# Kernel optimization log

Measured on AMD Instinct MI355X. Metric: run time of the kernel, lower is better.

## Reference

```python
import jax, jax.numpy as jnp
import numpy as np

T = 1000      # self.length in DMM
B = 16384     # batch
Z_DIM, X_DIM, H_DIM = 2, 3, 2
SIGMA = 0.01  # fixed scale used in both model and guide Normals
LOG2PI = float(np.log(2.0 * np.pi))


def _normal_logprob(x, mu, sigma):
    # elementwise Normal(mu, sigma).log_prob(x)
    return -0.5 * jnp.square((x - mu) / sigma) - jnp.log(sigma) - 0.5 * LOG2PI


def setup_inputs() -> dict:
    key = jax.random.key(0)
    ks = jax.random.split(key, 12)
    s = 0.3  # modest init scale for tiny linears
    return {
        "data": jax.random.normal(ks[0], (T, B, X_DIM), dtype=jnp.float32),
        "eps":  jax.random.normal(ks[1], (T, B, Z_DIM), dtype=jnp.float32),
        # guide RNN (Elman, tanh): input 3 -> hidden 2
        "W_ih": jax.random.normal(ks[2], (H_DIM, X_DIM), dtype=jnp.float32) * s,
        "W_hh": jax.random.normal(ks[3], (H_DIM, H_DIM), dtype=jnp.float32) * s,
        "b_ih": jax.random.normal(ks[4], (H_DIM,), dtype=jnp.float32) * s,
        "b_hh": jax.random.normal(ks[5], (H_DIM,), dtype=jnp.float32) * s,
        "h0":   jnp.zeros((H_DIM,), dtype=jnp.float32),   # nn.Parameter h_0
        "z0":   jnp.zeros((Z_DIM,), dtype=jnp.float32),   # nn.Parameter z_0
        # transition: Linear(2,2)
        "Wt": jax.random.normal(ks[6], (Z_DIM, Z_DIM), dtype=jnp.float32) * s,
        "bt": jax.random.normal(ks[7], (Z_DIM,), dtype=jnp.float32) * s,
        # emission: Linear(2,3)
        "We": jax.random.normal(ks[8], (X_DIM, Z_DIM), dtype=jnp.float32) * s,
        "be": jax.random.normal(ks[9], (X_DIM,), dtype=jnp.float32) * s,
    }


def reference(data, eps, W_ih, W_hh, b_ih, b_hh, h0, z0, Wt, bt, We, be):
    """Guide RNN + reparameterized latents + model log-joint minus guide log-prob.

    data: [T, B, 3], eps: [T, B, 2]. Returns scalar ELBO-style objective.
    """
    batch = data.shape[1]

    # --- guide: RNN over data (sequential recurrence, lax.scan) ---
    def step(h, x_t):
        h_new = jnp.tanh(x_t @ W_ih.T + b_ih + h @ W_hh.T + b_hh)
        return h_new, h_new

    h0b = jnp.broadcast_to(h0, (batch, H_DIM))
    _, rnn_out = jax.lax.scan(step, h0b, data)            # [T, B, 2]

    # z_t = Normal(rnn_out[t-1], SIGMA) sample, t = 1..T-1 (reparameterized)
    q_loc = rnn_out[:-1]                                   # [T-1, B, 2]
    z = q_loc + SIGMA * eps[1:]                            # [T-1, B, 2]

    # --- model: transition + emission over the latent chain ---
    z_prev = jnp.concatenate(
        [jnp.broadcast_to(z0, (1, batch, Z_DIM)), z[:-1]], axis=0)  # [T-1, B, 2]
    z_loc = z_prev @ Wt.T + bt                             # transition mean
    x_loc = z @ We.T + be                                  # emission mean [T-1, B, 3]

    logp = (_normal_logprob(z, z_loc, SIGMA).sum()
            + _normal_logprob(data[1:], x_loc, SIGMA).sum())
    logq = _normal_logprob(z, q_loc, SIGMA).sum()
    return logp - logq
```

## Files before the change

### kernel.cpp

```cpp
#include <hip/hip_runtime.h>

#define T_STEPS 1000
#define BATCH   16384

#define CH      40
#define NCHUNK  25
#define WARM    20
#define TT      4
#define BLK     256
#define NPART   (NCHUNK * (BATCH / BLK))

struct P {
    float w00,w01,w02,w10,w11,w12;
    float u00,u01,u10,u11,bs0,bs1;
    float wt00,wt01,wt10,wt11,bt0,bt1;
    float we00,we01,we10,we11,we20,we21,be0,be1,be2;
};

__device__ __forceinline__ float fast_tanh(float x) {
    float e = __expf(2.0f * x);
    return 1.0f - __fdividef(2.0f, e + 1.0f);
}

__device__ __forceinline__ void rnn_step(const P& p, float X0, float X1, float X2,
                                         float& h0, float& h1) {
    float p0 = p.bs0;
    p0 = __fmaf_rn(p.w00, X0, p0);
    p0 = __fmaf_rn(p.w01, X1, p0);
    p0 = __fmaf_rn(p.w02, X2, p0);
    p0 = __fmaf_rn(p.u00, h0, p0);
    p0 = __fmaf_rn(p.u01, h1, p0);
    float p1 = p.bs1;
    p1 = __fmaf_rn(p.w10, X0, p1);
    p1 = __fmaf_rn(p.w11, X1, p1);
    p1 = __fmaf_rn(p.w12, X2, p1);
    p1 = __fmaf_rn(p.u10, h0, p1);
    p1 = __fmaf_rn(p.u11, h1, p1);
    h0 = fast_tanh(p0);
    h1 = fast_tanh(p1);
}

__device__ __forceinline__ void body(const P& p, float X0, float X1, float X2,
                                     float E0, float E1,
                                     float& h0, float& h1, float& zp0, float& zp1,
                                     float& ssq, float& esq) {
    const float z0 = __fmaf_rn(0.01f, E0, h0);
    const float z1 = __fmaf_rn(0.01f, E1, h1);
    const float zl0 = __fmaf_rn(p.wt00, zp0, __fmaf_rn(p.wt01, zp1, p.bt0));
    const float zl1 = __fmaf_rn(p.wt10, zp0, __fmaf_rn(p.wt11, zp1, p.bt1));
    const float xl0 = __fmaf_rn(p.we00, z0, __fmaf_rn(p.we01, z1, p.be0));
    const float xl1 = __fmaf_rn(p.we10, z0, __fmaf_rn(p.we11, z1, p.be1));
    const float xl2 = __fmaf_rn(p.we20, z0, __fmaf_rn(p.we21, z1, p.be2));
    const float r0 = z0 - zl0;
    const float r1 = z1 - zl1;
    const float r2 = X0 - xl0;
    const float r3 = X1 - xl1;
    const float r4 = X2 - xl2;
    float s = r0 * r0;
    s = __fmaf_rn(r1, r1, s);
    s = __fmaf_rn(r2, r2, s);
    s = __fmaf_rn(r3, r3, s);
    s = __fmaf_rn(r4, r4, s);
    ssq += s;
    esq = __fmaf_rn(E0, E0, esq);
    esq = __fmaf_rn(E1, E1, esq);
    zp0 = z0; zp1 = z1;
    rnn_step(p, X0, X1, X2, h0, h1);
}

template<bool EPS_>
__device__ __forceinline__ void stage_tile(const float* __restrict__ data,
        const float* __restrict__ eps, float* db, float* ebf,
        int tbase, int b0, int w, int lane)
{
    const float4* srcd = reinterpret_cast<const float4*>(
        data + ((size_t)(tbase + w) * BATCH + b0) * 3);
    float4* dd = reinterpret_cast<float4*>(db + w * (BLK * 3));
    dd[lane]       = srcd[lane];
    dd[lane + 64]  = srcd[lane + 64];
    dd[lane + 128] = srcd[lane + 128];
    if constexpr (EPS_) {
        const float4* srce = reinterpret_cast<const float4*>(
            eps + ((size_t)(tbase + w) * BATCH + b0) * 2);
        float4* de = reinterpret_cast<float4*>(ebf + w * (BLK * 2));
        de[lane]      = srce[lane];
        de[lane + 64] = srce[lane + 64];
    }
}

template<int NW, bool TR, int NB>
__device__ __forceinline__ void compute_tile(const P& p, const float* db,
        const float* ebf, int tid,
        float& h0, float& h1, float& zp0, float& zp1, float& ssq, float& esq)
{
    const float* dp = db + tid * 3;
    const float2* ep = reinterpret_cast<const float2*>(ebf) + tid;
    int s = 0;
#pragma unroll
    for (int i = 0; i < NW; ++i, ++s)
        rnn_step(p, dp[s*BLK*3 + 0], dp[s*BLK*3 + 1], dp[s*BLK*3 + 2], h0, h1);
    if constexpr (TR) {
        const float2 E = ep[s * BLK];
        zp0 = __fmaf_rn(0.01f, E.x, h0);
        zp1 = __fmaf_rn(0.01f, E.y, h1);
        rnn_step(p, dp[s*BLK*3 + 0], dp[s*BLK*3 + 1], dp[s*BLK*3 + 2], h0, h1);
        ++s;
    }
#pragma unroll
    for (int i = 0; i < NB; ++i, ++s) {
        const float2 E = ep[s * BLK];
        body(p, dp[s*BLK*3 + 0], dp[s*BLK*3 + 1], dp[s*BLK*3 + 2],
             E.x, E.y, h0, h1, zp0, zp1, ssq, esq);
    }
}

template<int NT, int TRK, int TR_NW, int TR_NB, int EPS_FROM>
__device__ __forceinline__ void run_tiles(
    const float* __restrict__ data, const float* __restrict__ eps,
    float* dls0, float* dls1, float* els0, float* els1,
    int tb, int b0, int w, int lane, int tid, const P& p,
    float& h0, float& h1, float& zp0, float& zp1, float& ssq, float& esq)
{
    if (0 >= EPS_FROM) stage_tile<true >(data, eps, dls0, els0, tb, b0, w, lane);
    else               stage_tile<false>(data, eps, dls0, els0, tb, b0, w, lane);
    __syncthreads();
#pragma unroll
    for (int k = 0; k < NT; ++k) {
        float* dcur = (k & 1) ? dls1 : dls0;
        float* ecur = (k & 1) ? els1 : els0;
        float* dnxt = (k & 1) ? dls0 : dls1;
        float* enxt = (k & 1) ? els0 : els1;
        if (k + 1 < NT) {
            if ((k + 1) >= EPS_FROM)
                stage_tile<true >(data, eps, dnxt, enxt, tb + (k + 1) * TT, b0, w, lane);
            else
                stage_tile<false>(data, eps, dnxt, enxt, tb + (k + 1) * TT, b0, w, lane);
        }
        if (k < TRK)
            compute_tile<TT, false, 0>(p, dcur, ecur, tid, h0, h1, zp0, zp1, ssq, esq);
        else if (k == TRK)
            compute_tile<TR_NW, true, TR_NB>(p, dcur, ecur, tid, h0, h1, zp0, zp1, ssq, esq);
        else
            compute_tile<0, false, TT>(p, dcur, ecur, tid, h0, h1, zp0, zp1, ssq, esq);
        __syncthreads();
    }
}

__global__ __launch_bounds__(BLK, 2)
void elbo_kernel(const float* __restrict__ data,
                 const float* __restrict__ eps,
                 const float* __restrict__ W_ih,
                 const float* __restrict__ W_hh,
                 const float* __restrict__ b_ih,
                 const float* __restrict__ b_hh,
                 const float* __restrict__ h0p,
                 const float* __restrict__ z0p,
                 const float* __restrict__ Wt,
                 const float* __restrict__ bt,
                 const float* __restrict__ We,
                 const float* __restrict__ be,
                 float* __restrict__ partial)
{
    __shared__ float dls0[TT * BLK * 3], dls1[TT * BLK * 3];
    __shared__ float els0[TT * BLK * 2], els1[TT * BLK * 2];

    const int tid  = threadIdx.x;
    const int w    = tid >> 6;
    const int lane = tid & 63;
    const int b0   = blockIdx.x * BLK;
    const int b    = b0 + tid;
    const int c    = blockIdx.y;

    P p;
    p.w00 = W_ih[0]; p.w01 = W_ih[1]; p.w02 = W_ih[2];
    p.w10 = W_ih[3]; p.w11 = W_ih[4]; p.w12 = W_ih[5];
    p.u00 = W_hh[0]; p.u01 = W_hh[1]; p.u10 = W_hh[2]; p.u11 = W_hh[3];
    p.bs0 = b_ih[0] + b_hh[0];
    p.bs1 = b_ih[1] + b_hh[1];
    p.wt00 = Wt[0]; p.wt01 = Wt[1]; p.wt10 = Wt[2]; p.wt11 = Wt[3];
    p.bt0 = bt[0]; p.bt1 = bt[1];
    p.we00 = We[0]; p.we01 = We[1];
    p.we10 = We[2]; p.we11 = We[3];
    p.we20 = We[4]; p.we21 = We[5];
    p.be0 = be[0]; p.be1 = be[1]; p.be2 = be[2];

    float h0 = h0p[0], h1 = h0p[1];
    float zp0 = z0p[0], zp1 = z0p[1];
    float ssq = 0.0f, esq = 0.0f;

    if (c == 0) {
        const float* d0 = data + (size_t)b * 3;
        rnn_step(p, d0[0], d0[1], d0[2], h0, h1);
        run_tiles<10, -1, 0, 3, 0>(data, eps, dls0, dls1, els0, els1,
                                   1, b0, w, lane, tid, p, h0, h1, zp0, zp1, ssq, esq);
    } else if (c < NCHUNK - 1) {
        const int tp = c * CH - WARM;
        const float* dpr = data + ((size_t)tp * BATCH + b) * 3;
        rnn_step(p, dpr[0], dpr[1], dpr[2], h0, h1);
        run_tiles<15, 4, 3, 0, 4>(data, eps, dls0, dls1, els0, els1,
                                  tp + 1, b0, w, lane, tid, p, h0, h1, zp0, zp1, ssq, esq);
    } else {
        run_tiles<15, 5, 0, 3, 5>(data, eps, dls0, dls1, els0, els1,
                                  (NCHUNK - 1) * CH - WARM, b0, w, lane, tid, p,
                                  h0, h1, zp0, zp1, ssq, esq);
    }

    const int na = (c < NCHUNK - 1) ? CH : (T_STEPS - 1 - (NCHUNK - 1) * CH);
    const float CPT = (float)na * (3.0f * 3.6862316527806026f);
    float tval = __fmaf_rn(ssq, -5000.0f, __fmaf_rn(esq, 0.5f, CPT));

#pragma unroll
    for (int off = 32; off >= 1; off >>= 1)
        tval += __shfl_down(tval, off, 64);

    __shared__ float sm[BLK / 64];
    if ((tid & 63) == 0) sm[tid >> 6] = tval;
    __syncthreads();
    if (tid == 0) {
        float s = sm[0];
#pragma unroll
        for (int j = 1; j < BLK / 64; ++j) s += sm[j];
        partial[c * (BATCH / BLK) + blockIdx.x] = s;
    }
}

__global__ __launch_bounds__(256)
void reduce_kernel(const float* __restrict__ partial, float* __restrict__ out)
{
    float s = 0.0f;
    for (int i = threadIdx.x; i < NPART; i += 256)
        s += partial[i];
    __shared__ float sm[4];
#pragma unroll
    for (int off = 32; off >= 1; off >>= 1)
        s += __shfl_down(s, off, 64);
    if ((threadIdx.x & 63) == 0) sm[threadIdx.x >> 6] = s;
    __syncthreads();
    if (threadIdx.x == 0)
        out[0] = sm[0] + sm[1] + sm[2] + sm[3];
}

extern "C" void kernel_launch(void* const* d_in, const int* in_sizes, int n_in,
                              void* d_out, int out_size, void* d_ws, size_t ws_size,
                              hipStream_t stream) {
    const float* data = (const float*)d_in[0];
    const float* eps  = (const float*)d_in[1];
    const float* W_ih = (const float*)d_in[2];
    const float* W_hh = (const float*)d_in[3];
    const float* b_ih = (const float*)d_in[4];
    const float* b_hh = (const float*)d_in[5];
    const float* h0   = (const float*)d_in[6];
    const float* z0   = (const float*)d_in[7];
    const float* Wt   = (const float*)d_in[8];
    const float* bt   = (const float*)d_in[9];
    const float* We   = (const float*)d_in[10];
    const float* be   = (const float*)d_in[11];
    float* out     = (float*)d_out;
    float* partial = (float*)d_ws;

    elbo_kernel<<<dim3(BATCH / BLK, NCHUNK), dim3(BLK), 0, stream>>>(
        data, eps, W_ih, W_hh, b_ih, b_hh, h0, z0, Wt, bt, We, be, partial);
    reduce_kernel<<<dim3(1), dim3(256), 0, stream>>>(partial, out);
}
```

Baseline: 382.7 us.

## Prefetch next tile into registers and write LDS after compute; raise occupancy

Replaces the fully unrolled, templated per-chunk tile loop with a single runtime loop. The next tile's global loads go into registers before the current tile is computed, and are written to shared memory only after compute. This lets global load latency hide behind compute instead of stalling on the direct global-to-LDS copy. The change also raises launch_bounds min blocks from 2 to 3 and merges the three code paths to cut code size. In exchange it adds staging registers, a runtime-branching transition tile, and a tighter register budget that could cause spills.

```diff
diff --git a/kernel.cpp b/kernel.cpp
--- a/kernel.cpp
+++ b/kernel.cpp
@@ -68,85 +68,90 @@
     rnn_step(p, X0, X1, X2, h0, h1);
 }
 
-template<bool EPS_>
-__device__ __forceinline__ void stage_tile(const float* __restrict__ data,
-        const float* __restrict__ eps, float* db, float* ebf,
-        int tbase, int b0, int w, int lane)
+struct Stg {
+    float4 d0, d1, d2;
+    float4 e0, e1;
+};
+
+__device__ __forceinline__ void stage_load(const float* __restrict__ data,
+        const float* __restrict__ eps, Stg& r,
+        int tbase, int b0, int w, int lane, bool do_eps)
 {
     const float4* srcd = reinterpret_cast<const float4*>(
         data + ((size_t)(tbase + w) * BATCH + b0) * 3);
-    float4* dd = reinterpret_cast<float4*>(db + w * (BLK * 3));
-    dd[lane]       = srcd[lane];
-    dd[lane + 64]  = srcd[lane + 64];
-    dd[lane + 128] = srcd[lane + 128];
-    if constexpr (EPS_) {
+    r.d0 = srcd[lane];
+    r.d1 = srcd[lane + 64];
+    r.d2 = srcd[lane + 128];
+    if (do_eps) {
         const float4* srce = reinterpret_cast<const float4*>(
             eps + ((size_t)(tbase + w) * BATCH + b0) * 2);
+        r.e0 = srce[lane];
+        r.e1 = srce[lane + 64];
+    }
+}
+
+__device__ __forceinline__ void stage_write(float* db, float* ebf, const Stg& r,
+        int w, int lane, bool do_eps)
+{
+    float4* dd = reinterpret_cast<float4*>(db + w * (BLK * 3));
+    dd[lane]       = r.d0;
+    dd[lane + 64]  = r.d1;
+    dd[lane + 128] = r.d2;
+    if (do_eps) {
         float4* de = reinterpret_cast<float4*>(ebf + w * (BLK * 2));
-        de[lane]      = srce[lane];
-        de[lane + 64] = srce[lane + 64];
-    }
-}
-
-template<int NW, bool TR, int NB>
-__device__ __forceinline__ void compute_tile(const P& p, const float* db,
+        de[lane]      = r.e0;
+        de[lane + 64] = r.e1;
+    }
+}
+
+__device__ __forceinline__ void compute_warm4(const P& p, const float* db, int tid,
+        float& h0, float& h1)
+{
+    const float* dp = db + tid * 3;
+#pragma unroll
+    for (int s = 0; s < TT; ++s)
+        rnn_step(p, dp[s*BLK*3 + 0], dp[s*BLK*3 + 1], dp[s*BLK*3 + 2], h0, h1);
+}
+
+__device__ __forceinline__ void compute_body4(const P& p, const float* db,
         const float* ebf, int tid,
         float& h0, float& h1, float& zp0, float& zp1, float& ssq, float& esq)
 {
     const float* dp = db + tid * 3;
     const float2* ep = reinterpret_cast<const float2*>(ebf) + tid;
-    int s = 0;
-#pragma unroll
-    for (int i = 0; i < NW; ++i, ++s)
-        rnn_step(p, dp[s*BLK*3 + 0], dp[s*BLK*3 + 1], dp[s*BLK*3 + 2], h0, h1);
-    if constexpr (TR) {
-        const float2 E = ep[s * BLK];
-        zp0 = __fmaf_rn(0.01f, E.x, h0);
-        zp1 = __fmaf_rn(0.01f, E.y, h1);
-        rnn_step(p, dp[s*BLK*3 + 0], dp[s*BLK*3 + 1], dp[s*BLK*3 + 2], h0, h1);
-        ++s;
-    }
-#pragma unroll
-    for (int i = 0; i < NB; ++i, ++s) {
+#pragma unroll
+    for (int s = 0; s < TT; ++s) {
         const float2 E = ep[s * BLK];
         body(p, dp[s*BLK*3 + 0], dp[s*BLK*3 + 1], dp[s*BLK*3 + 2],
              E.x, E.y, h0, h1, zp0, zp1, ssq, esq);
     }
 }
 
-template<int NT, int TRK, int TR_NW, int TR_NB, int EPS_FROM>
-__device__ __forceinline__ void run_tiles(
-    const float* __restrict__ data, const float* __restrict__ eps,
-    float* dls0, float* dls1, float* els0, float* els1,
-    int tb, int b0, int w, int lane, int tid, const P& p,
-    float& h0, float& h1, float& zp0, float& zp1, float& ssq, float& esq)
-{
-    if (0 >= EPS_FROM) stage_tile<true >(data, eps, dls0, els0, tb, b0, w, lane);
-    else               stage_tile<false>(data, eps, dls0, els0, tb, b0, w, lane);
-    __syncthreads();
-#pragma unroll
-    for (int k = 0; k < NT; ++k) {
-        float* dcur = (k & 1) ? dls1 : dls0;
-        float* ecur = (k & 1) ? els1 : els0;
-        float* dnxt = (k & 1) ? dls0 : dls1;
-        float* enxt = (k & 1) ? els0 : els1;
-        if (k + 1 < NT) {
-            if ((k + 1) >= EPS_FROM)
-                stage_tile<true >(data, eps, dnxt, enxt, tb + (k + 1) * TT, b0, w, lane);
-            else
-                stage_tile<false>(data, eps, dnxt, enxt, tb + (k + 1) * TT, b0, w, lane);
+__device__ __forceinline__ void compute_tr(const P& p, const float* db,
+        const float* ebf, int tid, int nw,
+        float& h0, float& h1, float& zp0, float& zp1, float& ssq, float& esq)
+{
+    const float* dp = db + tid * 3;
+    const float2* ep = reinterpret_cast<const float2*>(ebf) + tid;
+    for (int s = 0; s < TT; ++s) {
+        const float X0 = dp[s*BLK*3 + 0];
+        const float X1 = dp[s*BLK*3 + 1];
+        const float X2 = dp[s*BLK*3 + 2];
+        if (s < nw) {
+            rnn_step(p, X0, X1, X2, h0, h1);
+        } else if (s == nw) {
+            const float2 E = ep[s * BLK];
+            zp0 = __fmaf_rn(0.01f, E.x, h0);
+            zp1 = __fmaf_rn(0.01f, E.y, h1);
+            rnn_step(p, X0, X1, X2, h0, h1);
+        } else {
+            const float2 E = ep[s * BLK];
+            body(p, X0, X1, X2, E.x, E.y, h0, h1, zp0, zp1, ssq, esq);
         }
-        if (k < TRK)
-            compute_tile<TT, false, 0>(p, dcur, ecur, tid, h0, h1, zp0, zp1, ssq, esq);
-        else if (k == TRK)
-            compute_tile<TR_NW, true, TR_NB>(p, dcur, ecur, tid, h0, h1, zp0, zp1, ssq, esq);
-        else
-            compute_tile<0, false, TT>(p, dcur, ecur, tid, h0, h1, zp0, zp1, ssq, esq);
-        __syncthreads();
-    }
-}
-
-__global__ __launch_bounds__(BLK, 2)
+    }
+}
+
+__global__ __launch_bounds__(BLK, 3)
 void elbo_kernel(const float* __restrict__ data,
                  const float* __restrict__ eps,
                  const float* __restrict__ W_ih,
@@ -188,21 +193,47 @@
     float zp0 = z0p[0], zp1 = z0p[1];
     float ssq = 0.0f, esq = 0.0f;
 
+    if (c < NCHUNK - 1) {
+        const int tpre = (c == 0) ? 0 : c * CH - WARM;
+        const float* dpr = data + ((size_t)tpre * BATCH + b) * 3;
+        rnn_step(p, dpr[0], dpr[1], dpr[2], h0, h1);
+    }
+
+    int tb, nt, trk, trnw, eps_from;
     if (c == 0) {
-        const float* d0 = data + (size_t)b * 3;
-        rnn_step(p, d0[0], d0[1], d0[2], h0, h1);
-        run_tiles<10, -1, 0, 3, 0>(data, eps, dls0, dls1, els0, els1,
-                                   1, b0, w, lane, tid, p, h0, h1, zp0, zp1, ssq, esq);
+        tb = 1;                         nt = 10; trk = -1; trnw = 0; eps_from = 0;
     } else if (c < NCHUNK - 1) {
-        const int tp = c * CH - WARM;
-        const float* dpr = data + ((size_t)tp * BATCH + b) * 3;
-        rnn_step(p, dpr[0], dpr[1], dpr[2], h0, h1);
-        run_tiles<15, 4, 3, 0, 4>(data, eps, dls0, dls1, els0, els1,
-                                  tp + 1, b0, w, lane, tid, p, h0, h1, zp0, zp1, ssq, esq);
+        tb = c * CH - WARM + 1;         nt = 15; trk = 4;  trnw = 3; eps_from = 4;
     } else {
-        run_tiles<15, 5, 0, 3, 5>(data, eps, dls0, dls1, els0, els1,
-                                  (NCHUNK - 1) * CH - WARM, b0, w, lane, tid, p,
-                                  h0, h1, zp0, zp1, ssq, esq);
+        tb = (NCHUNK - 1) * CH - WARM;  nt = 15; trk = 5;  trnw = 0; eps_from = 5;
+    }
+
+    {
+        Stg r;
+        stage_load(data, eps, r, tb, b0, w, lane, 0 >= eps_from);
+        stage_write(dls0, els0, r, w, lane, 0 >= eps_from);
+        __syncthreads();
+
+        float* dcur = dls0; float* ecur = els0;
+        float* dnxt = dls1; float* enxt = els1;
+#pragma unroll 1
+        for (int k = 0; k < nt; ++k) {
+            const bool pf = (k + 1 < nt);
+            const bool pe = (k + 1 >= eps_from);
+            if (pf) stage_load(data, eps, r, tb + (k + 1) * TT, b0, w, lane, pe);
+
+            if (k < trk)
+                compute_warm4(p, dcur, tid, h0, h1);
+            else if (k == trk)
+                compute_tr(p, dcur, ecur, tid, trnw, h0, h1, zp0, zp1, ssq, esq);
+            else
+                compute_body4(p, dcur, ecur, tid, h0, h1, zp0, zp1, ssq, esq);
+
+            if (pf) stage_write(dnxt, enxt, r, w, lane, pe);
+            __syncthreads();
+            float* td = dcur; dcur = dnxt; dnxt = td;
+            float* te = ecur; ecur = enxt; enxt = te;
+        }
     }
 
     const int na = (c < NCHUNK - 1) ? CH : (T_STEPS - 1 - (NCHUNK - 1) * CH);
```

Result: slower. 453.8 us (+18.6%).
